# Kernel tuning notes

Measured on AMD Instinct MI355X. Metric: run time of the kernel, lower is better.

The kernel has to match this reference:

```python
import jax, jax.numpy as jnp
import numpy as np

B, N, C_IN, C_OUT = 8, 4096, 64, 64
NEG_INF = -9e15
LEAKY_SLOPE = 0.01  # torch F.leaky_relu default


def setup_inputs() -> dict:
    key = jax.random.key(0)
    kx, ka, kw, kq, kk = jax.random.split(key, 5)
    X = jax.random.normal(kx, (B, N, C_IN), dtype=jnp.float32)
    A = jax.random.randint(ka, (N, N), 0, 2, dtype=jnp.int32)
    # xavier_uniform with gain=1.414 ~ scaled uniform; plain scaled normal is fine for a numeric reference
    def xavier(k, shape):
        fan_in, fan_out = shape
        bound = 1.414 * np.sqrt(6.0 / (fan_in + fan_out))
        return jax.random.uniform(k, shape, jnp.float32, -bound, bound)
    weight = xavier(kw, (C_IN, C_OUT))
    query = xavier(kq, (C_IN, C_OUT))
    key_p = xavier(kk, (C_IN, C_OUT))
    return {"X": X, "A": A, "weight": weight, "query": query, "key_p": key_p}


def reference(X, A, weight, query, key_p):
    n = X.shape[1]
    idx = jnp.arange(n)
    adj = A.at[idx, idx].set(1)  # add self-loops
    out = jnp.einsum('bni,io->bno', X, weight)
    q = jnp.einsum('bni,io->bno', X, query)
    k = jnp.einsum('bni,io->bno', X, key_p)
    att = jnp.einsum('bnd,bmd->bnm', q, k)          # QK^T, (B,N,N)
    att = jax.nn.leaky_relu(att, LEAKY_SLOPE)
    att = jnp.where(adj[None, :, :] > 0, att, NEG_INF)
    att = jax.nn.softmax(att, axis=-1)
    # dropout p=0 and/or eval mode -> identity
    return jnp.einsum('bnm,bmo->bno', att, out)
```

## Files before the change

kernel.cpp:

```cpp
#include <hip/hip_runtime.h>
#include <stdint.h>

#define BATCH 8
#define NN 4096
#define CC 64
#define MASKV -1.0e30f
#define LOG2E 1.4426950408889634f

typedef _Float16 half8 __attribute__((ext_vector_type(8)));
typedef __fp16 fp16x2 __attribute__((ext_vector_type(2)));
typedef float f32x4 __attribute__((ext_vector_type(4)));

__global__ __launch_bounds__(256) void gat_proj(
    const float* __restrict__ X, const float* __restrict__ W0,
    const float* __restrict__ Wq, const float* __restrict__ Wk,
    _Float16* __restrict__ qh, _Float16* __restrict__ ql,
    _Float16* __restrict__ kb, _Float16* __restrict__ vt)
{
    __shared__ alignas(16) _Float16 WTh[3][64][72];
    __shared__ alignas(16) _Float16 WTl[3][64][72];
    const int t = threadIdx.x;
    const float* Ws[3] = {W0, Wq, Wk};
    for (int e = t; e < 4096; e += 256) {
        int k = e >> 6, c = e & 63;
        #pragma unroll
        for (int m = 0; m < 3; ++m) {
            float w = Ws[m][e];
            _Float16 hi = (_Float16)w;
            WTh[m][c][k] = hi;
            WTl[m][c][k] = (_Float16)(w - (float)hi);
        }
    }
    __syncthreads();
    const int lane = t & 63, wv = t >> 6;
    const int cl = lane & 15, g = lane >> 4;
    {
        int tile = blockIdx.x * 4 + wv;
        int gr = tile * 16;
        const float* xr = X + (size_t)(gr + cl) * CC;
        half8 xh[2], xl[2];
        #pragma unroll
        for (int kf = 0; kf < 2; ++kf) {
            f32x4 a0 = *(const f32x4*)(xr + g*8 + kf*32);
            f32x4 a1 = *(const f32x4*)(xr + g*8 + kf*32 + 4);
            half8 h, l;
            #pragma unroll
            for (int j = 0; j < 4; ++j) {
                _Float16 h0 = (_Float16)a0[j], h1 = (_Float16)a1[j];
                h[j]   = h0; l[j]   = (_Float16)(a0[j] - (float)h0);
                h[j+4] = h1; l[j+4] = (_Float16)(a1[j] - (float)h1);
            }
            xh[kf] = h; xl[kf] = l;
        }
        #pragma unroll
        for (int mat = 1; mat <= 2; ++mat) {
            #pragma unroll
            for (int nt = 0; nt < 4; ++nt) {
                f32x4 acc = {0.f, 0.f, 0.f, 0.f};
                #pragma unroll
                for (int kf = 0; kf < 2; ++kf) {
                    half8 bh = *(const half8*)&WTh[mat][nt*16 + cl][g*8 + kf*32];
                    half8 bl = *(const half8*)&WTl[mat][nt*16 + cl][g*8 + kf*32];
                    acc = __builtin_amdgcn_mfma_f32_16x16x32_f16(xh[kf], bh, acc, 0, 0, 0);
                    acc = __builtin_amdgcn_mfma_f32_16x16x32_f16(xl[kf], bh, acc, 0, 0, 0);
                    acc = __builtin_amdgcn_mfma_f32_16x16x32_f16(xh[kf], bl, acc, 0, 0, 0);
                }
                #pragma unroll
                for (int i = 0; i < 4; ++i) {
                    size_t off = (size_t)(gr + 4*g + i) * CC + nt*16 + cl;
                    if (mat == 1) {
                        float qs = acc[i] * LOG2E;
                        _Float16 hi = (_Float16)qs;
                        qh[off] = hi;
                        ql[off] = (_Float16)(qs - (float)hi);
                    } else {
                        kb[off] = (_Float16)acc[i];
                    }
                }
            }
        }
        {
            int b = gr >> 12, n0 = gr & (NN - 1);
            #pragma unroll
            for (int mt = 0; mt < 4; ++mt) {
                f32x4 acc = {0.f, 0.f, 0.f, 0.f};
                #pragma unroll
                for (int kf = 0; kf < 2; ++kf) {
                    half8 ah = *(const half8*)&WTh[0][mt*16 + cl][g*8 + kf*32];
                    half8 al = *(const half8*)&WTl[0][mt*16 + cl][g*8 + kf*32];
                    acc = __builtin_amdgcn_mfma_f32_16x16x32_f16(ah, xh[kf], acc, 0, 0, 0);
                    acc = __builtin_amdgcn_mfma_f32_16x16x32_f16(al, xh[kf], acc, 0, 0, 0);
                    acc = __builtin_amdgcn_mfma_f32_16x16x32_f16(ah, xl[kf], acc, 0, 0, 0);
                }
                #pragma unroll
                for (int i = 0; i < 4; ++i) {
                    int co = mt*16 + 4*g + i;
                    vt[((size_t)b * CC + co) * NN + n0 + cl] = (_Float16)acc[i];
                }
            }
        }
    }
}

__global__ __launch_bounds__(256) void gat_mask(const int* __restrict__ A,
                                                uint4* __restrict__ AM)
{
    const int r = blockIdx.x;
    const int t = threadIdx.x;
    const int kc = t >> 2, g = t & 3;
    unsigned w[4];
    #pragma unroll
    for (int kt = 0; kt < 4; ++kt) {
        const int k0 = kc*64 + kt*16 + 4*g;
        int4 a = *(const int4*)(A + (size_t)r * NN + k0);
        unsigned m = 0;
        m |= (a.x != 0 || k0     == r) ? 0x000000FFu : 0u;
        m |= (a.y != 0 || k0 + 1 == r) ? 0x0000FF00u : 0u;
        m |= (a.z != 0 || k0 + 2 == r) ? 0x00FF0000u : 0u;
        m |= (a.w != 0 || k0 + 3 == r) ? 0xFF000000u : 0u;
        w[kt] = m;
    }
    AM[(size_t)r * 256 + t] = make_uint4(w[0], w[1], w[2], w[3]);
}

__global__ __launch_bounds__(256) void gat_attn(
    const _Float16* __restrict__ qh, const _Float16* __restrict__ ql,
    const _Float16* __restrict__ kf16, const _Float16* __restrict__ vtb,
    const uint4* __restrict__ AM,
    _Float16* __restrict__ po, float2* __restrict__ pml)
{
    __shared__ alignas(16) _Float16 Kt[64][64];
    __shared__ alignas(16) _Float16 Vt[64][64];
    __shared__ alignas(16) _Float16 Ps[4][32][64];
    const int t = threadIdx.x;
    const int lane = t & 63, wv = t >> 6;
    const int cl = lane & 15, g = lane >> 4;
    const int blk = blockIdx.x;
    const int b  = blk & 7;
    const int sp = (blk >> 3) & 3;
    const int qb = blk >> 5;
    const int Q0 = qb * 128 + wv * 32;
    const int c0 = sp * 16;
    const int swz = (cl & 7) << 4;

    const int soff = (((t >> 3) * 128 + (t & 7) * 16) ^ (((t >> 3) & 7) << 4));
    char* const kd0 = (char*)Kt + soff;
    char* const kd1 = (char*)Kt + soff + 32 * 128;
    char* const vd0 = (char*)Vt + soff;
    char* const vd1 = (char*)Vt + soff + 32 * 128;
    char* const psb = (char*)&Ps[wv][0][0];

    half8 qfh[2][2], qfl[2][2];
    #pragma unroll
    for (int qt = 0; qt < 2; ++qt) {
        const _Float16* qrh = qh + ((size_t)b * NN + Q0 + qt*16 + cl) * CC;
        const _Float16* qrl = ql + ((size_t)b * NN + Q0 + qt*16 + cl) * CC;
        qfh[qt][0] = *(const half8*)(qrh + g*8);
        qfh[qt][1] = *(const half8*)(qrh + g*8 + 32);
        qfl[qt][0] = *(const half8*)(qrl + g*8);
        qfl[qt][1] = *(const half8*)(qrl + g*8 + 32);
    }
    const _Float16* kg = kf16 + (size_t)b * NN * CC;
    const _Float16* vg = vtb + (size_t)b * CC * NN;

    f32x4 o[2][4] = {};
    float m_run[2] = {MASKV, MASKV}, l_run[2] = {0.f, 0.f};

    uint4 pk0, pk1, pv0, pv1, pa, pb;
    auto loadchunk = [&](int kc) {
        const uint4* ks = (const uint4*)(kg + (size_t)kc * 64 * CC);
        pk0 = ks[t];
        pk1 = ks[t + 256];
        const _Float16* vs = vg + kc * 64;
        pv0 = *(const uint4*)(vs + (size_t)(t >> 3) * NN + (t & 7) * 8);
        pv1 = *(const uint4*)(vs + (size_t)((t >> 3) + 32) * NN + (t & 7) * 8);
        pa = AM[(size_t)(Q0 + cl)      * 256 + kc * 4 + g];
        pb = AM[(size_t)(Q0 + 16 + cl) * 256 + kc * 4 + g];
    };
    loadchunk(c0);

    auto pkmax = [](unsigned a, unsigned b) {
        unsigned d;
        asm("v_pk_max_f16 %0, %1, %2" : "=v"(d) : "v"(a), "v"(b));
        return d;
    };

    for (int kc = 0; kc < 16; ++kc) {
        __syncthreads();
        *(uint4*)kd0 = pk0;
        *(uint4*)kd1 = pk1;
        *(uint4*)vd0 = pv0;
        *(uint4*)vd1 = pv1;
        const uint4 ca = pa, cb = pb;
        __syncthreads();
        if (kc < 15) loadchunk(c0 + kc + 1);

        __builtin_amdgcn_s_setprio(1);
        f32x4 sc[2][4] = {};
        #pragma unroll
        for (int kt = 0; kt < 4; ++kt) {
            #pragma unroll
            for (int kf = 0; kf < 2; ++kf) {
                half8 ka = *(const half8*)((char*)Kt +
                    ((((kt*16 + cl) * 128) + g*16 + kf*64) ^ swz));
                sc[0][kt] = __builtin_amdgcn_mfma_f32_16x16x32_f16(ka, qfh[0][kf], sc[0][kt], 0, 0, 0);
                sc[0][kt] = __builtin_amdgcn_mfma_f32_16x16x32_f16(ka, qfl[0][kf], sc[0][kt], 0, 0, 0);
                sc[1][kt] = __builtin_amdgcn_mfma_f32_16x16x32_f16(ka, qfh[1][kf], sc[1][kt], 0, 0, 0);
                sc[1][kt] = __builtin_amdgcn_mfma_f32_16x16x32_f16(ka, qfl[1][kf], sc[1][kt], 0, 0, 0);
            }
        }
        __builtin_amdgcn_s_setprio(0);

        #pragma unroll
        for (int qt = 0; qt < 2; ++qt) {
            const uint4 wm = qt ? cb : ca;
            const unsigned am[4] = {wm.x, wm.y, wm.z, wm.w};
            unsigned hm[8];
            #pragma unroll
            for (int kt = 0; kt < 4; ++kt) {
                hm[2*kt]   = __builtin_amdgcn_perm(0u, am[kt], 0x01010000u);
                hm[2*kt+1] = __builtin_amdgcn_perm(0u, am[kt], 0x03030202u);
            }
            float sv[16];
            #pragma unroll
            for (int j = 0; j < 16; ++j) {
                float x = sc[qt][j >> 2][j & 3];
                sv[j] = fmaxf(x, 0.01f * x);
            }
            union UH { unsigned u; fp16x2 h; };
            unsigned sm[8];
            #pragma unroll
            for (int kt = 0; kt < 4; ++kt) {
                UH s0, s1;
                s0.h = __builtin_amdgcn_cvt_pkrtz(sv[4*kt + 0], sv[4*kt + 1]);
                s1.h = __builtin_amdgcn_cvt_pkrtz(sv[4*kt + 2], sv[4*kt + 3]);
                sm[2*kt]   = (hm[2*kt]   & s0.u) | (~hm[2*kt]   & 0xFC00FC00u);
                sm[2*kt+1] = (hm[2*kt+1] & s1.u) | (~hm[2*kt+1] & 0xFC00FC00u);
            }
            unsigned tm = pkmax(
                pkmax(pkmax(sm[0], sm[1]), pkmax(sm[2], sm[3])),
                pkmax(pkmax(sm[4], sm[5]), pkmax(sm[6], sm[7])));
            UH tmu; tmu.u = tm;
            float mx = fmaxf((float)tmu.h[0], (float)tmu.h[1]);
            mx = fmaxf(mx, __shfl_xor(mx, 16));
            mx = fmaxf(mx, __shfl_xor(mx, 32));
            if (__any(mx > m_run[qt])) {
                float nm = fmaxf(m_run[qt], mx);
                float alpha = __builtin_amdgcn_exp2f(m_run[qt] - nm);
                m_run[qt] = nm;
                l_run[qt] *= alpha;
                #pragma unroll
                for (int ct = 0; ct < 4; ++ct) o[qt][ct] *= alpha;
            }
            float p[16];
            #pragma unroll
            for (int j = 0; j < 16; ++j)
                p[j] = __builtin_amdgcn_exp2f(sv[j] - m_run[qt]);
            UH zz; zz.u = 0u;
            fp16x2 acc2 = zz.h;
            #pragma unroll
            for (int kt = 0; kt < 4; ++kt) {
                UH w0, w1;
                w0.h = __builtin_amdgcn_cvt_pkrtz(p[kt*4 + 0], p[kt*4 + 1]);
                w1.h = __builtin_amdgcn_cvt_pkrtz(p[kt*4 + 2], p[kt*4 + 3]);
                w0.u &= hm[2*kt];
                w1.u &= hm[2*kt+1];
                uint2 pw = {w0.u, w1.u};
                *(uint2*)(psb + ((((qt*16 + cl) * 128) + kt*32 + g*8) ^ swz)) = pw;
                acc2 += w0.h + w1.h;
            }
            l_run[qt] += (float)acc2[0] + (float)acc2[1];
        }
        __builtin_amdgcn_wave_barrier();

        half8 pf[2][2];
        #pragma unroll
        for (int qt = 0; qt < 2; ++qt) {
            pf[qt][0] = *(const half8*)(psb + ((((qt*16 + cl) * 128) + g*16) ^ swz));
            pf[qt][1] = *(const half8*)(psb + ((((qt*16 + cl) * 128) + g*16 + 64) ^ swz));
        }
        __builtin_amdgcn_s_setprio(1);
        #pragma unroll
        for (int ct = 0; ct < 4; ++ct) {
            half8 vf0 = *(const half8*)((char*)Vt + ((((ct*16 + cl) * 128) + g*16) ^ swz));
            half8 vf1 = *(const half8*)((char*)Vt + ((((ct*16 + cl) * 128) + g*16 + 64) ^ swz));
            #pragma unroll
            for (int qt = 0; qt < 2; ++qt) {
                o[qt][ct] = __builtin_amdgcn_mfma_f32_16x16x32_f16(vf0, pf[qt][0], o[qt][ct], 0, 0, 0);
                o[qt][ct] = __builtin_amdgcn_mfma_f32_16x16x32_f16(vf1, pf[qt][1], o[qt][ct], 0, 0, 0);
            }
        }
        __builtin_amdgcn_s_setprio(0);
    }

    #pragma unroll
    for (int qt = 0; qt < 2; ++qt) {
        float lt = l_run[qt];
        lt += __shfl_xor(lt, 16);
        lt += __shfl_xor(lt, 32);
        size_t base = (size_t)sp * (BATCH * NN) + (size_t)b * NN + Q0 + qt*16 + cl;
        _Float16* orow = po + base * 64;
        #pragma unroll
        for (int ct = 0; ct < 4; ++ct) {
            union { fp16x2 h; unsigned u; } o0u, o1u;
            o0u.h = __builtin_amdgcn_cvt_pkrtz(o[qt][ct][0], o[qt][ct][1]);
            o1u.h = __builtin_amdgcn_cvt_pkrtz(o[qt][ct][2], o[qt][ct][3]);
            uint2 ow = {o0u.u, o1u.u};
            *(uint2*)(orow + ct*16 + 4*g) = ow;
        }
        if (g == 0) pml[base] = make_float2(m_run[qt], lt);
    }
}

__global__ __launch_bounds__(256) void gat_comb(
    const _Float16* __restrict__ po, const float2* __restrict__ pml,
    float* __restrict__ out)
{
    int gid = blockIdx.x * 256 + threadIdx.x;
    int row = gid >> 2;
    int col = (gid & 3) * 16;
    float2 ml[4];
    float Mx = MASKV;
    #pragma unroll
    for (int s = 0; s < 4; ++s) {
        ml[s] = pml[s * (BATCH * NN) + row];
        Mx = fmaxf(Mx, ml[s].x);
    }
    float w[4], den = 0.f;
    #pragma unroll
    for (int s = 0; s < 4; ++s) {
        w[s] = __builtin_amdgcn_exp2f(ml[s].x - Mx);
        den += w[s] * ml[s].y;
    }
    float inv = 1.0f / den;
    float acc[16] = {};
    #pragma unroll
    for (int s = 0; s < 4; ++s) {
        const _Float16* p = po + ((size_t)s * (BATCH * NN) + row) * 64 + col;
        float a = w[s] * inv;
        half8 v0 = *(const half8*)(p);
        half8 v1 = *(const half8*)(p + 8);
        #pragma unroll
        for (int j = 0; j < 8; ++j) {
            acc[j]     += a * (float)v0[j];
            acc[j + 8] += a * (float)v1[j];
        }
    }
    float* op = out + (size_t)row * 64 + col;
    #pragma unroll
    for (int i = 0; i < 4; ++i) {
        f32x4 r = {acc[4*i], acc[4*i+1], acc[4*i+2], acc[4*i+3]};
        *(f32x4*)(op + i*4) = r;
    }
}

extern "C" void kernel_launch(void* const* d_in, const int* in_sizes, int n_in,
                              void* d_out, int out_size, void* d_ws, size_t ws_size,
                              hipStream_t stream) {
    const float* X  = (const float*)d_in[0];
    const int*   A  = (const int*)d_in[1];
    const float* W0 = (const float*)d_in[2];
    const float* Wq = (const float*)d_in[3];
    const float* Wk = (const float*)d_in[4];
    float* out = (float*)d_out;
    char* ws = (char*)d_ws;
    const size_t SZ = (size_t)BATCH * NN * CC * 2;
    _Float16* qh  = (_Float16*)(ws);
    _Float16* ql  = (_Float16*)(ws + SZ);
    _Float16* kbf = (_Float16*)(ws + 2*SZ);
    _Float16* vtb = (_Float16*)(ws + 3*SZ);
    uint4* AMp    = (uint4*)(ws + 4*SZ);
    _Float16* po  = (_Float16*)(ws + 4*SZ + (size_t)16*1024*1024);
    float2* pml   = (float2*)(ws + 4*SZ + (size_t)32*1024*1024);

    hipLaunchKernelGGL(gat_proj, dim3(512),  dim3(256), 0, stream, X, W0, Wq, Wk, qh, ql, kbf, vtb);
    hipLaunchKernelGGL(gat_mask, dim3(4096), dim3(256), 0, stream, A, AMp);
    hipLaunchKernelGGL(gat_attn, dim3(1024), dim3(256), 0, stream, qh, ql, kbf, vtb,
                       AMp, po, pml);
    hipLaunchKernelGGL(gat_comb, dim3(512),  dim3(256), 0, stream, po, pml, out);
}
```

Before: 209.6 us.

## Pack adjacency mask to 1 bit per entry and expand via LDS lookup table

Changes the precomputed adjacency mask from a byte per entry (16 MB) to a bit per entry (2 MB). The mask kernel writes 16-bit words and the attention kernel loads one 64-bit word per row per chunk. It rebuilds the half-precision select masks from nibbles through a small shared-memory lookup table. This cuts mask write and read traffic, at the cost of extra shifts and LDS lookups in the attention inner loop.

```diff
diff --git a/kernel.cpp b/kernel.cpp
--- a/kernel.cpp
+++ b/kernel.cpp
@@ -103,35 +103,34 @@
 }
 
 __global__ __launch_bounds__(256) void gat_mask(const int* __restrict__ A,
-                                                uint4* __restrict__ AM)
+                                                unsigned short* __restrict__ M16)
 {
-    const int r = blockIdx.x;
-    const int t = threadIdx.x;
-    const int kc = t >> 2, g = t & 3;
-    unsigned w[4];
-    #pragma unroll
-    for (int kt = 0; kt < 4; ++kt) {
-        const int k0 = kc*64 + kt*16 + 4*g;
-        int4 a = *(const int4*)(A + (size_t)r * NN + k0);
-        unsigned m = 0;
-        m |= (a.x != 0 || k0     == r) ? 0x000000FFu : 0u;
-        m |= (a.y != 0 || k0 + 1 == r) ? 0x0000FF00u : 0u;
-        m |= (a.z != 0 || k0 + 2 == r) ? 0x00FF0000u : 0u;
-        m |= (a.w != 0 || k0 + 3 == r) ? 0xFF000000u : 0u;
-        w[kt] = m;
-    }
-    AM[(size_t)r * 256 + t] = make_uint4(w[0], w[1], w[2], w[3]);
+    const int row = blockIdx.x;
+    const int w16 = threadIdx.x;
+    const int4* ap = (const int4*)(A + (size_t)row * NN + w16 * 16);
+    unsigned m = 0;
+    #pragma unroll
+    for (int j = 0; j < 4; ++j) {
+        int4 a = ap[j];
+        m |= (a.x != 0 ? 1u : 0u) << (4*j);
+        m |= (a.y != 0 ? 1u : 0u) << (4*j + 1);
+        m |= (a.z != 0 ? 1u : 0u) << (4*j + 2);
+        m |= (a.w != 0 ? 1u : 0u) << (4*j + 3);
+    }
+    if (w16 == (row >> 4)) m |= 1u << (row & 15);
+    M16[(size_t)row * 256 + w16] = (unsigned short)m;
 }
 
 __global__ __launch_bounds__(256) void gat_attn(
     const _Float16* __restrict__ qh, const _Float16* __restrict__ ql,
     const _Float16* __restrict__ kf16, const _Float16* __restrict__ vtb,
-    const uint4* __restrict__ AM,
+    const unsigned long long* __restrict__ M,
     _Float16* __restrict__ po, float2* __restrict__ pml)
 {
     __shared__ alignas(16) _Float16 Kt[64][64];
     __shared__ alignas(16) _Float16 Vt[64][64];
     __shared__ alignas(16) _Float16 Ps[4][32][64];
+    __shared__ alignas(8) uint2 LUT[16];
     const int t = threadIdx.x;
     const int lane = t & 63, wv = t >> 6;
     const int cl = lane & 15, g = lane >> 4;
@@ -143,6 +142,12 @@
     const int c0 = sp * 16;
     const int swz = (cl & 7) << 4;
 
+    if (t < 16) {
+        unsigned n = t;
+        LUT[n] = make_uint2(((n & 1u) ? 0x0000FFFFu : 0u) | ((n & 2u) ? 0xFFFF0000u : 0u),
+                            ((n & 4u) ? 0x0000FFFFu : 0u) | ((n & 8u) ? 0xFFFF0000u : 0u));
+    }
+
     const int soff = (((t >> 3) * 128 + (t & 7) * 16) ^ (((t >> 3) & 7) << 4));
     char* const kd0 = (char*)Kt + soff;
     char* const kd1 = (char*)Kt + soff + 32 * 128;
@@ -166,7 +171,8 @@
     f32x4 o[2][4] = {};
     float m_run[2] = {MASKV, MASKV}, l_run[2] = {0.f, 0.f};
 
-    uint4 pk0, pk1, pv0, pv1, pa, pb;
+    uint4 pk0, pk1, pv0, pv1;
+    unsigned long long pmA, pmB;
     auto loadchunk = [&](int kc) {
         const uint4* ks = (const uint4*)(kg + (size_t)kc * 64 * CC);
         pk0 = ks[t];
@@ -174,8 +180,8 @@
         const _Float16* vs = vg + kc * 64;
         pv0 = *(const uint4*)(vs + (size_t)(t >> 3) * NN + (t & 7) * 8);
         pv1 = *(const uint4*)(vs + (size_t)((t >> 3) + 32) * NN + (t & 7) * 8);
-        pa = AM[(size_t)(Q0 + cl)      * 256 + kc * 4 + g];
-        pb = AM[(size_t)(Q0 + 16 + cl) * 256 + kc * 4 + g];
+        pmA = M[(size_t)(Q0 + cl) * 64 + kc];
+        pmB = M[(size_t)(Q0 + 16 + cl) * 64 + kc];
     };
     loadchunk(c0);
 
@@ -191,7 +197,7 @@
         *(uint4*)kd1 = pk1;
         *(uint4*)vd0 = pv0;
         *(uint4*)vd1 = pv1;
-        const uint4 ca = pa, cb = pb;
+        const unsigned long long cmA = pmA, cmB = pmB;
         __syncthreads();
         if (kc < 15) loadchunk(c0 + kc + 1);
 
@@ -213,13 +219,16 @@
 
         #pragma unroll
         for (int qt = 0; qt < 2; ++qt) {
-            const uint4 wm = qt ? cb : ca;
-            const unsigned am[4] = {wm.x, wm.y, wm.z, wm.w};
+            const unsigned long long cm = qt ? cmB : cmA;
+            const unsigned wlo = (unsigned)cm, whi = (unsigned)(cm >> 32);
             unsigned hm[8];
             #pragma unroll
             for (int kt = 0; kt < 4; ++kt) {
-                hm[2*kt]   = __builtin_amdgcn_perm(0u, am[kt], 0x01010000u);
-                hm[2*kt+1] = __builtin_amdgcn_perm(0u, am[kt], 0x03030202u);
+                unsigned w = (kt < 2) ? wlo : whi;
+                unsigned nib = (w >> ((kt & 1) * 16 + 4 * g)) & 15u;
+                uint2 e = LUT[nib];
+                hm[2*kt]   = e.x;
+                hm[2*kt+1] = e.y;
             }
             float sv[16];
             #pragma unroll
@@ -369,13 +378,13 @@
     _Float16* ql  = (_Float16*)(ws + SZ);
     _Float16* kbf = (_Float16*)(ws + 2*SZ);
     _Float16* vtb = (_Float16*)(ws + 3*SZ);
-    uint4* AMp    = (uint4*)(ws + 4*SZ);
-    _Float16* po  = (_Float16*)(ws + 4*SZ + (size_t)16*1024*1024);
-    float2* pml   = (float2*)(ws + 4*SZ + (size_t)32*1024*1024);
+    char* Mbase = ws + 4*SZ;
+    _Float16* po = (_Float16*)(Mbase + 2*1024*1024);
+    float2* pml  = (float2*)(Mbase + 2*1024*1024 + 4*SZ);
 
     hipLaunchKernelGGL(gat_proj, dim3(512),  dim3(256), 0, stream, X, W0, Wq, Wk, qh, ql, kbf, vtb);
-    hipLaunchKernelGGL(gat_mask, dim3(4096), dim3(256), 0, stream, A, AMp);
+    hipLaunchKernelGGL(gat_mask, dim3(4096), dim3(256), 0, stream, A, (unsigned short*)Mbase);
     hipLaunchKernelGGL(gat_attn, dim3(1024), dim3(256), 0, stream, qh, ql, kbf, vtb,
-                       AMp, po, pml);
+                       (const unsigned long long*)Mbase, po, pml);
     hipLaunchKernelGGL(gat_comb, dim3(512),  dim3(256), 0, stream, po, pml, out);
 }
```

Measured after the change: 205.7 us. No clear change (-1.9%).
